# Performance work log

Hardware: AMD Instinct MI355X
Metric: run time of the kernel (lower is better)

The kernel has to match this reference:

```python
import jax, jax.numpy as jnp
import numpy as np

DIM = 1024
NUM_HEAD = 16
DIM_HEAD = DIM // NUM_HEAD
RMS_EPS = 1.1920929e-07  # torch.finfo(float32).eps (nn.RMSNorm default eps=None)
EPS_LIN = 1e-6
THETA = 10000.0


def rmsnorm(x, g, eps=RMS_EPS):
    return x * jax.lax.rsqrt(jnp.mean(x * x, axis=-1, keepdims=True) + eps) * g


def rope_cos_sin(seq_len, dim_head, dtype=jnp.float32):
    inv_freq = 1.0 / (THETA ** (jnp.arange(0, dim_head, 2, dtype=dtype) / dim_head))
    t = jnp.arange(seq_len, dtype=dtype)
    freqs = jnp.outer(t, inv_freq)  # [L, dh//2]
    return jnp.cos(freqs), jnp.sin(freqs)


def apply_rope(t, cos, sin):
    # t: [b, h, L, dh]; pairs are (t[...,2i], t[...,2i+1]) viewed as complex
    tr = t[..., 0::2]
    ti = t[..., 1::2]
    out_r = tr * cos - ti * sin
    out_i = tr * sin + ti * cos
    return jnp.stack([out_r, out_i], axis=-1).reshape(t.shape)


def setup_inputs() -> dict:
    key = jax.random.key(0)
    ks = jax.random.split(key, 5)
    B, L = 4, 4096
    x = jax.random.normal(ks[0], (B, L, DIM), dtype=jnp.float32)
    Wqkv = jax.random.normal(ks[1], (3 * DIM, DIM), dtype=jnp.float32) * 0.02
    bqkv = jax.random.normal(ks[2], (3 * DIM,), dtype=jnp.float32) * 0.02
    gq = jnp.ones((DIM,), dtype=jnp.float32)
    gk = jnp.ones((DIM,), dtype=jnp.float32)
    Wout = jax.random.normal(ks[3], (DIM, DIM), dtype=jnp.float32) * 0.02
    bout = jax.random.normal(ks[4], (DIM,), dtype=jnp.float32) * 0.02
    gout = jnp.ones((DIM,), dtype=jnp.float32)
    return {"x": x, "Wqkv": Wqkv, "bqkv": bqkv, "gq": gq, "gk": gk,
            "Wout": Wout, "bout": bout, "gout": gout}


def reference(x, Wqkv, bqkv, gq, gk, Wout, bout, gout):
    B, L, D = x.shape
    qkv = x @ Wqkv.T + bqkv  # [B, L, 3D]
    q, k, v = jnp.split(qkv, 3, axis=-1)
    q = rmsnorm(q, gq)
    k = rmsnorm(k, gk)
    # b L (h d) -> b h L d
    split = lambda t: t.reshape(B, L, NUM_HEAD, DIM_HEAD).transpose(0, 2, 1, 3)
    q, k, v = split(q), split(k), split(v)
    cos, sin = rope_cos_sin(L, DIM_HEAD)  # start_pos = 0 (default)
    cos = cos[None, None]  # [1,1,L,dh//2]
    sin = sin[None, None]
    q = apply_rope(q, cos, sin)
    k = apply_rope(k, cos, sin)
    # linear attention: ReLU feature map + padded-value normalization trick
    qf = jax.nn.relu(q)
    kf = jax.nn.relu(k)
    vpad = jnp.concatenate([v, jnp.ones_like(v[..., :1])], axis=-1)  # pad_val=1.0
    vk = jnp.einsum('bhlp,bhld->bhpd', vpad, kf)       # [b,h,dh+1,dh]
    res = jnp.einsum('bhpd,bhld->bhlp', vk, qf)        # [b,h,L,dh+1]
    attn = res[..., :-1] / (res[..., -1:] + EPS_LIN)
    attn = attn.transpose(0, 2, 1, 3).reshape(B, L, D)  # b h L d -> b L (h d)
    out = rmsnorm(attn @ Wout.T + bout, gout)
    return out
```

## Files before the change

kernel.cpp:

```cpp
#include <hip/hip_runtime.h>
#include <stdint.h>

#define RMS_EPS 1.1920929e-07f
#define EPS_LIN 1e-6f

typedef __attribute__((ext_vector_type(8))) short bf16x8;
typedef __attribute__((ext_vector_type(4))) float f32x4;

__device__ __forceinline__ unsigned short f2bf(float f) {
  union { float f; unsigned int u; } v; v.f = f;
  unsigned int r = v.u + 0x7fffu + ((v.u >> 16) & 1u);
  return (unsigned short)(r >> 16);
}
__device__ __forceinline__ float bf2f(unsigned short s) {
  union { unsigned int u; float f; } v; v.u = ((unsigned int)s) << 16;
  return v.f;
}

__global__ __launch_bounds__(256) void k_init(
    const float* __restrict__ x, const float* __restrict__ Wqkv,
    const float* __restrict__ Wout,
    unsigned short* __restrict__ xb, unsigned short* __restrict__ wqkvb,
    unsigned short* __restrict__ woutb,
    float* __restrict__ cosT, float* __restrict__ sinT,
    float* __restrict__ vkbuf) {
  const int blk = blockIdx.x;
  const int t = threadIdx.x;
  if (blk < 20480) {
    const float* src;
    unsigned short* dst;
    int base;
    if (blk < 16384) { src = x; dst = xb; base = blk; }
    else if (blk < 19456) { src = Wqkv; dst = wqkvb; base = blk - 16384; }
    else { src = Wout; dst = woutb; base = blk - 19456; }
    int i = (base * 256 + t) * 4;
    float4 v = *reinterpret_cast<const float4*>(src + i);
    ushort4 o = { f2bf(v.x), f2bf(v.y), f2bf(v.z), f2bf(v.w) };
    *reinterpret_cast<ushort4*>(dst + i) = o;
  } else if (blk < 20992) {
    int idx = (blk - 20480) * 256 + t;
    int l = idx >> 5, i = idx & 31;
    float inv_freq = expf(-((float)(2 * i) / 64.0f) * logf(10000.0f));
    float ang = (float)l * inv_freq;
    cosT[idx] = cosf(ang);
    sinT[idx] = sinf(ang);
  } else {
    int i = ((blk - 20992) * 256 + t) * 4;
    if (i < 64 * 65 * 64) {
      float4 z = { 0.f, 0.f, 0.f, 0.f };
      *reinterpret_cast<float4*>(vkbuf + i) = z;
    }
  }
}

__device__ __forceinline__ void stage16(const unsigned short* g, unsigned short* lds_base,
                                        int lane) {
#if __has_builtin(__builtin_amdgcn_global_load_lds)
  __builtin_amdgcn_global_load_lds(
      (const __attribute__((address_space(1))) unsigned int*)g,
      (__attribute__((address_space(3))) unsigned int*)lds_base, 16, 0, 0);
#else
  *reinterpret_cast<uint4*>(lds_base + lane * 8) = *reinterpret_cast<const uint4*>(g);
#endif
}

__global__ __launch_bounds__(256, 3) void k_gemm_bt(
    const unsigned short* __restrict__ A, const unsigned short* __restrict__ Bw,
    const float* __restrict__ bias, int M, int N, int K, int mode,
    unsigned short* __restrict__ qb, unsigned short* __restrict__ kb,
    unsigned short* __restrict__ vb, unsigned short* __restrict__ preb) {
  __shared__ unsigned short As[128 * 64];
  __shared__ unsigned short Bs[128 * 64];
  const int nt = N >> 7;
  const int bm = blockIdx.x / nt, bn = blockIdx.x % nt;
  const int m0 = bm << 7, n0 = bn << 7;
  const int t = threadIdx.x;
  const int wave = t >> 6, lane = t & 63;
  const int wr = wave >> 1, wc = wave & 1;
  const int quad = lane >> 4, m16 = lane & 15;

  const unsigned short* ApS[4];
  const unsigned short* BpS[4];
  unsigned short* AlS[4];
  unsigned short* BlS[4];
#pragma unroll
  for (int s = 0; s < 4; ++s) {
    int u = wave * 256 + s * 64 + lane;
    int row = u >> 3;
    int ku = (u & 7) ^ (row & 7);
    ApS[s] = A + (size_t)(m0 + row) * K + ku * 8;
    BpS[s] = Bw + (size_t)(n0 + row) * K + ku * 8;
    AlS[s] = As + (size_t)(wave * 256 + s * 64) * 8;
    BlS[s] = Bs + (size_t)(wave * 256 + s * 64) * 8;
  }

  int offA[4][2], offB[4][2];
#pragma unroll
  for (int i = 0; i < 4; ++i) {
    int rowA = wr * 64 + i * 16 + m16;
    int rowB = wc * 64 + i * 16 + m16;
#pragma unroll
    for (int ks = 0; ks < 2; ++ks) {
      int kuf = ks * 4 + quad;
      offA[i][ks] = (rowA * 8 + (kuf ^ (rowA & 7))) * 8;
      offB[i][ks] = (rowB * 8 + (kuf ^ (rowB & 7))) * 8;
    }
  }

  f32x4 acc[4][4] = {};

  for (int k0 = 0; k0 < K; k0 += 64) {
#pragma unroll
    for (int s = 0; s < 4; ++s) {
      stage16(ApS[s] + k0, AlS[s], lane);
      stage16(BpS[s] + k0, BlS[s], lane);
    }
    __syncthreads();
#pragma unroll
    for (int ks = 0; ks < 2; ++ks) {
      bf16x8 fa[4], fb[4];
#pragma unroll
      for (int i = 0; i < 4; ++i)
        fa[i] = *reinterpret_cast<const bf16x8*>(As + offA[i][ks]);
#pragma unroll
      for (int j = 0; j < 4; ++j)
        fb[j] = *reinterpret_cast<const bf16x8*>(Bs + offB[j][ks]);
#pragma unroll
      for (int i = 0; i < 4; ++i)
#pragma unroll
        for (int j = 0; j < 4; ++j)
          acc[i][j] = __builtin_amdgcn_mfma_f32_16x16x32_bf16(fa[i], fb[j], acc[i][j], 0, 0, 0);
    }
    __syncthreads();
  }

#pragma unroll
  for (int i = 0; i < 4; ++i) {
    int rbase = m0 + wr * 64 + i * 16 + quad * 4;
#pragma unroll
    for (int j = 0; j < 4; ++j) {
      int col = n0 + wc * 64 + j * 16 + m16;
      float bc = bias[col];
#pragma unroll
      for (int r = 0; r < 4; ++r) {
        int row = rbase + r;
        float val = acc[i][j][r] + bc;
        unsigned short bv = f2bf(val);
        if (mode == 0) {
          if (col < 1024) {
            qb[(size_t)row * 1024 + col] = bv;
          } else if (col < 2048) {
            kb[(size_t)row * 1024 + (col - 1024)] = bv;
          } else {
            int h = (col - 2048) >> 6, d = col & 63;
            int b = row >> 12, l = row & 4095;
            vb[(((size_t)(b * 16 + h)) * 4096 + l) * 64 + d] = bv;
          }
        } else {
          preb[(size_t)row * N + col] = bv;
        }
      }
    }
  }
}

__global__ __launch_bounds__(256) void k_qknorm(
    const unsigned short* __restrict__ qb, const unsigned short* __restrict__ kb,
    const float* __restrict__ gq, const float* __restrict__ gk,
    const float* __restrict__ cosT, const float* __restrict__ sinT,
    unsigned short* __restrict__ qfb, unsigned short* __restrict__ kfb) {
  const int wid = (blockIdx.x << 2) + (threadIdx.x >> 6);
  const int row = wid >> 1;
  const int which = wid & 1;
  const int lane = threadIdx.x & 63;
  const int l = row & 4095;
  const int b = row >> 12;
  const unsigned short* src = (which ? kb : qb) + (size_t)row * 1024;
  const float* g = which ? gk : gq;
  unsigned short* dstb = which ? kfb : qfb;

  float v[16];
  float ss = 0.f;
#pragma unroll
  for (int c = 0; c < 4; ++c) {
    int d = c * 256 + lane * 4;
    ushort4 u = *reinterpret_cast<const ushort4*>(src + d);
    float a0 = bf2f(u.x), a1 = bf2f(u.y), a2 = bf2f(u.z), a3 = bf2f(u.w);
    v[c * 4 + 0] = a0; v[c * 4 + 1] = a1; v[c * 4 + 2] = a2; v[c * 4 + 3] = a3;
    ss += a0 * a0 + a1 * a1 + a2 * a2 + a3 * a3;
  }
#pragma unroll
  for (int off = 1; off < 64; off <<= 1) ss += __shfl_xor(ss, off, 64);
  const float sc = rsqrtf(ss * (1.0f / 1024.0f) + RMS_EPS);

#pragma unroll
  for (int c = 0; c < 4; ++c) {
    int d = c * 256 + lane * 4;
    int i0 = (d & 63) >> 1;
    float c0 = cosT[l * 32 + i0], s0 = sinT[l * 32 + i0];
    float c1 = cosT[l * 32 + i0 + 1], s1 = sinT[l * 32 + i0 + 1];
    float x0 = v[c * 4 + 0] * sc * g[d];
    float x1 = v[c * 4 + 1] * sc * g[d + 1];
    float x2 = v[c * 4 + 2] * sc * g[d + 2];
    float x3 = v[c * 4 + 3] * sc * g[d + 3];
    float r0 = x0 * c0 - x1 * s0, r1 = x0 * s0 + x1 * c0;
    float r2 = x2 * c1 - x3 * s1, r3 = x2 * s1 + x3 * c1;
    ushort4 o = { f2bf(fmaxf(r0, 0.f)), f2bf(fmaxf(r1, 0.f)),
                  f2bf(fmaxf(r2, 0.f)), f2bf(fmaxf(r3, 0.f)) };
    int h = d >> 6;
    *reinterpret_cast<ushort4*>(dstb + (((size_t)(b * 16 + h)) * 4096 + l) * 64 + (d & 63)) = o;
  }
}

__global__ __launch_bounds__(256) void k_vk(const unsigned short* __restrict__ vb,
                                            const unsigned short* __restrict__ kfb,
                                            float* __restrict__ vk) {
  const int bh = blockIdx.x >> 4;
  const int chunk = blockIdx.x & 15;
  const int t = threadIdx.x;
  const int wv = t >> 6, tx = t & 63;
  __shared__ float vt[64 * 64];
  __shared__ float kt[64 * 64];
  float acc[16] = {};
  float accD = 0.f;
  const int lb = chunk * 256;
  for (int tile = 0; tile < 4; ++tile) {
    const size_t rowbase = ((size_t)bh * 4096 + lb + tile * 64) * 64;
#pragma unroll
    for (int r = 0; r < 4; ++r) {
      int e = r * 1024 + t * 4;
      ushort4 uv = *reinterpret_cast<const ushort4*>(vb + rowbase + e);
      ushort4 uk = *reinterpret_cast<const ushort4*>(kfb + rowbase + e);
      float4 fv = { bf2f(uv.x), bf2f(uv.y), bf2f(uv.z), bf2f(uv.w) };
      float4 fk = { bf2f(uk.x), bf2f(uk.y), bf2f(uk.z), bf2f(uk.w) };
      *reinterpret_cast<float4*>(vt + e) = fv;
      *reinterpret_cast<float4*>(kt + e) = fk;
    }
    __syncthreads();
#pragma unroll 4
    for (int lp = 0; lp < 64; ++lp) {
      float kvv = kt[lp * 64 + tx];
      const float4* vr = reinterpret_cast<const float4*>(vt + lp * 64 + wv * 16);
      float4 v0 = vr[0], v1 = vr[1], v2 = vr[2], v3 = vr[3];
      acc[0] += v0.x * kvv;  acc[1] += v0.y * kvv;
      acc[2] += v0.z * kvv;  acc[3] += v0.w * kvv;
      acc[4] += v1.x * kvv;  acc[5] += v1.y * kvv;
      acc[6] += v1.z * kvv;  acc[7] += v1.w * kvv;
      acc[8] += v2.x * kvv;  acc[9] += v2.y * kvv;
      acc[10] += v2.z * kvv; acc[11] += v2.w * kvv;
      acc[12] += v3.x * kvv; acc[13] += v3.y * kvv;
      acc[14] += v3.z * kvv; acc[15] += v3.w * kvv;
      accD += kvv;
    }
    __syncthreads();
  }
  float* dst = vk + (size_t)bh * 65 * 64;
#pragma unroll
  for (int pp = 0; pp < 16; ++pp) atomicAdd(dst + (wv * 16 + pp) * 64 + tx, acc[pp]);
  if (wv == 0) atomicAdd(dst + 64 * 64 + tx, accD);
}

__global__ __launch_bounds__(256) void k_res(const unsigned short* __restrict__ qfb,
                                             const float* __restrict__ vk,
                                             unsigned short* __restrict__ attnb) {
  const int bh = blockIdx.x >> 5;
  const int lt = (blockIdx.x & 31) << 7;
  const int b = bh >> 4, h = bh & 15;
  const int t = threadIdx.x;
  const int wave = t >> 6, lane = t & 63;
  __shared__ unsigned short Aq[128 * 64];
  __shared__ unsigned short Bv[64 * 64];
  __shared__ float vkD[64];
  __shared__ float invden[128];

  const unsigned short* Ag = qfb + ((size_t)bh * 4096 + lt) * 64;
#pragma unroll
  for (int s = 0; s < 4; ++s)
    stage16(Ag + wave * 2048 + s * 512 + lane * 8, Aq + wave * 2048 + s * 512, lane);

  const float* vsrc = vk + (size_t)bh * 65 * 64;
  {
    int base = t * 16;
#pragma unroll
    for (int c = 0; c < 4; ++c) {
      float4 f = *reinterpret_cast<const float4*>(vsrc + base + c * 4);
      ushort4 o = { f2bf(f.x), f2bf(f.y), f2bf(f.z), f2bf(f.w) };
      *reinterpret_cast<ushort4*>(Bv + base + c * 4) = o;
    }
  }
  if (t < 64) vkD[t] = vsrc[64 * 64 + t];
  __syncthreads();

  f32x4 acc[2][4] = {};
  const int quad = lane >> 4, m16 = lane & 15;
#pragma unroll
  for (int step = 0; step < 2; ++step) {
    bf16x8 fa[2], fb[4];
#pragma unroll
    for (int i = 0; i < 2; ++i)
      fa[i] = *reinterpret_cast<const bf16x8*>(Aq + (wave * 32 + i * 16 + m16) * 64 +
                                               step * 32 + quad * 8);
#pragma unroll
    for (int j = 0; j < 4; ++j)
      fb[j] = *reinterpret_cast<const bf16x8*>(Bv + (j * 16 + m16) * 64 +
                                               step * 32 + quad * 8);
#pragma unroll
    for (int i = 0; i < 2; ++i)
#pragma unroll
      for (int j = 0; j < 4; ++j)
        acc[i][j] = __builtin_amdgcn_mfma_f32_16x16x32_bf16(fa[i], fb[j], acc[i][j], 0, 0, 0);
  }

  {
    const unsigned short* qr = Aq + (t >> 1) * 64 + (t & 1) * 32;
    const float* vd = vkD + (t & 1) * 32;
    float ds = 0.f;
#pragma unroll
    for (int c = 0; c < 4; ++c) {
      bf16x8 qv = *reinterpret_cast<const bf16x8*>(qr + c * 8);
#pragma unroll
      for (int j = 0; j < 8; ++j)
        ds += bf2f((unsigned short)qv[j]) * vd[c * 8 + j];
    }
    ds += __shfl_xor(ds, 1, 64);
    if ((t & 1) == 0) invden[t >> 1] = 1.0f / (ds + EPS_LIN);
  }
  __syncthreads();

#pragma unroll
  for (int i = 0; i < 2; ++i) {
#pragma unroll
    for (int r = 0; r < 4; ++r) {
      int row = wave * 32 + i * 16 + quad * 4 + r;
      float inv = invden[row];
      unsigned short* dst = attnb + ((size_t)(b * 4096 + lt + row)) * 1024 + h * 64;
#pragma unroll
      for (int j = 0; j < 4; ++j)
        dst[j * 16 + m16] = f2bf(acc[i][j][r] * inv);
    }
  }
}

__global__ __launch_bounds__(256) void k_outnorm(const unsigned short* __restrict__ preb,
                                                 const float* __restrict__ gout,
                                                 float* __restrict__ out) {
  const int row = (blockIdx.x << 2) + (threadIdx.x >> 6);
  const int lane = threadIdx.x & 63;
  const unsigned short* src = preb + (size_t)row * 1024;
  float* drow = out + (size_t)row * 1024;
  float v[16];
  float ss = 0.f;
#pragma unroll
  for (int c = 0; c < 4; ++c) {
    int d = c * 256 + lane * 4;
    ushort4 u = *reinterpret_cast<const ushort4*>(src + d);
    float a0 = bf2f(u.x), a1 = bf2f(u.y), a2 = bf2f(u.z), a3 = bf2f(u.w);
    v[c * 4 + 0] = a0; v[c * 4 + 1] = a1; v[c * 4 + 2] = a2; v[c * 4 + 3] = a3;
    ss += a0 * a0 + a1 * a1 + a2 * a2 + a3 * a3;
  }
#pragma unroll
  for (int off = 1; off < 64; off <<= 1) ss += __shfl_xor(ss, off, 64);
  const float sc = rsqrtf(ss * (1.0f / 1024.0f) + RMS_EPS);
#pragma unroll
  for (int c = 0; c < 4; ++c) {
    int d = c * 256 + lane * 4;
    float4 o = { v[c * 4 + 0] * sc * gout[d], v[c * 4 + 1] * sc * gout[d + 1],
                 v[c * 4 + 2] * sc * gout[d + 2], v[c * 4 + 3] * sc * gout[d + 3] };
    *reinterpret_cast<float4*>(drow + d) = o;
  }
}

#define OFF_XB     0ull
#define OFF_WQKVB  33554432ull
#define OFF_WOUTB  39845888ull
#define OFF_QB     41943040ull
#define OFF_KB     75497472ull
#define OFF_VB     109051904ull
#define OFF_QFB    142606336ull
#define OFF_KFB    176160768ull
#define OFF_VK     209715200ull
#define OFF_ATTNB  210780160ull
#define OFF_COST   244334592ull
#define OFF_SINT   244858880ull
#define WS_NEEDED  245383168ull

extern "C" void kernel_launch(void* const* d_in, const int* in_sizes, int n_in,
                              void* d_out, int out_size, void* d_ws, size_t ws_size,
                              hipStream_t stream) {
  const float* x    = (const float*)d_in[0];
  const float* Wqkv = (const float*)d_in[1];
  const float* bqkv = (const float*)d_in[2];
  const float* gq   = (const float*)d_in[3];
  const float* gk   = (const float*)d_in[4];
  const float* Wout = (const float*)d_in[5];
  const float* bout = (const float*)d_in[6];
  const float* gout = (const float*)d_in[7];

  if (ws_size < WS_NEEDED) return;

  char* ws = (char*)d_ws;
  unsigned short* xb    = (unsigned short*)(ws + OFF_XB);
  unsigned short* wqkvb = (unsigned short*)(ws + OFF_WQKVB);
  unsigned short* woutb = (unsigned short*)(ws + OFF_WOUTB);
  unsigned short* qb    = (unsigned short*)(ws + OFF_QB);
  unsigned short* kb    = (unsigned short*)(ws + OFF_KB);
  unsigned short* vb    = (unsigned short*)(ws + OFF_VB);
  unsigned short* qfb   = (unsigned short*)(ws + OFF_QFB);
  unsigned short* kfb   = (unsigned short*)(ws + OFF_KFB);
  float*          vkbuf = (float*)(ws + OFF_VK);
  unsigned short* attnb = (unsigned short*)(ws + OFF_ATTNB);
  float*          cosT  = (float*)(ws + OFF_COST);
  float*          sinT  = (float*)(ws + OFF_SINT);
  unsigned short* preb  = (unsigned short*)(ws + OFF_QB);

  k_init<<<21252, 256, 0, stream>>>(x, Wqkv, Wout, xb, wqkvb, woutb, cosT, sinT, vkbuf);

  k_gemm_bt<<<128 * 24, 256, 0, stream>>>(xb, wqkvb, bqkv, 16384, 3072, 1024, 0,
                                          qb, kb, vb, nullptr);
  k_qknorm<<<8192, 256, 0, stream>>>(qb, kb, gq, gk, cosT, sinT, qfb, kfb);

  k_vk<<<1024, 256, 0, stream>>>(vb, kfb, vkbuf);
  k_res<<<2048, 256, 0, stream>>>(qfb, vkbuf, attnb);

  k_gemm_bt<<<128 * 8, 256, 0, stream>>>(attnb, woutb, bout, 16384, 1024, 1024, 1,
                                         nullptr, nullptr, nullptr, preb);
  k_outnorm<<<4096, 256, 0, stream>>>(preb, gout, (float*)d_out);
}
```

Baseline: 395.1 us.

## Restructure vk reduction into per-wave 8x8 register outer-product tiles

The k_vk kernel now gives each wave its own slice of sequence rows. Each lane accumulates an 8x8 register tile of the V^T·K outer product, fed by vectorized LDS loads, instead of a 16x1 strip per thread. Partial tiles from the four waves are summed in shared memory before global atomics, so each block issues fewer atomic adds. The grid is halved, so each block covers 512 rows. This trades more registers per thread and an extra LDS reduction pass for higher arithmetic intensity per LDS load.

```diff
diff --git a/kernel.cpp b/kernel.cpp
--- a/kernel.cpp
+++ b/kernel.cpp
@@ -212,52 +212,99 @@
   }
 }
 
+__device__ __forceinline__ float4 lo4(uint4 u) {
+  union { unsigned int v; float f; } a0, a1, b0, b1;
+  a0.v = u.x << 16; a1.v = u.x & 0xffff0000u;
+  b0.v = u.y << 16; b1.v = u.y & 0xffff0000u;
+  float4 r = { a0.f, a1.f, b0.f, b1.f };
+  return r;
+}
+__device__ __forceinline__ float4 hi4(uint4 u) {
+  union { unsigned int v; float f; } a0, a1, b0, b1;
+  a0.v = u.z << 16; a1.v = u.z & 0xffff0000u;
+  b0.v = u.w << 16; b1.v = u.w & 0xffff0000u;
+  float4 r = { a0.f, a1.f, b0.f, b1.f };
+  return r;
+}
+
 __global__ __launch_bounds__(256) void k_vk(const unsigned short* __restrict__ vb,
                                             const unsigned short* __restrict__ kfb,
                                             float* __restrict__ vk) {
-  const int bh = blockIdx.x >> 4;
-  const int chunk = blockIdx.x & 15;
+  const int bh = blockIdx.x >> 3;
+  const int chunk = blockIdx.x & 7;
   const int t = threadIdx.x;
-  const int wv = t >> 6, tx = t & 63;
-  __shared__ float vt[64 * 64];
-  __shared__ float kt[64 * 64];
-  float acc[16] = {};
-  float accD = 0.f;
-  const int lb = chunk * 256;
-  for (int tile = 0; tile < 4; ++tile) {
-    const size_t rowbase = ((size_t)bh * 4096 + lb + tile * 64) * 64;
-#pragma unroll
-    for (int r = 0; r < 4; ++r) {
-      int e = r * 1024 + t * 4;
-      ushort4 uv = *reinterpret_cast<const ushort4*>(vb + rowbase + e);
-      ushort4 uk = *reinterpret_cast<const ushort4*>(kfb + rowbase + e);
-      float4 fv = { bf2f(uv.x), bf2f(uv.y), bf2f(uv.z), bf2f(uv.w) };
-      float4 fk = { bf2f(uk.x), bf2f(uk.y), bf2f(uk.z), bf2f(uk.w) };
-      *reinterpret_cast<float4*>(vt + e) = fv;
-      *reinterpret_cast<float4*>(kt + e) = fk;
+  const int wv = t >> 6, lane = t & 63;
+  const int p0 = (lane >> 3) << 3, d0 = (lane & 7) << 3;
+  __shared__ float sh[16384];
+  float* vt = sh + wv * 2048;
+  float* kt = sh + 8192 + wv * 2048;
+
+  float acc[8][8] = {};
+  float accD[8] = {};
+
+  for (int it = 0; it < 4; ++it) {
+    const int l0 = (chunk * 16 + wv * 4 + it) * 32;
+    const size_t base = ((size_t)bh * 4096 + l0) * 64;
+#pragma unroll
+    for (int c = 0; c < 4; ++c) {
+      const int e = c * 512 + lane * 8;
+      uint4 uv = *reinterpret_cast<const uint4*>(vb + base + e);
+      uint4 uk = *reinterpret_cast<const uint4*>(kfb + base + e);
+      *reinterpret_cast<float4*>(vt + e) = lo4(uv);
+      *reinterpret_cast<float4*>(vt + e + 4) = hi4(uv);
+      *reinterpret_cast<float4*>(kt + e) = lo4(uk);
+      *reinterpret_cast<float4*>(kt + e + 4) = hi4(uk);
     }
     __syncthreads();
-#pragma unroll 4
-    for (int lp = 0; lp < 64; ++lp) {
-      float kvv = kt[lp * 64 + tx];
-      const float4* vr = reinterpret_cast<const float4*>(vt + lp * 64 + wv * 16);
-      float4 v0 = vr[0], v1 = vr[1], v2 = vr[2], v3 = vr[3];
-      acc[0] += v0.x * kvv;  acc[1] += v0.y * kvv;
-      acc[2] += v0.z * kvv;  acc[3] += v0.w * kvv;
-      acc[4] += v1.x * kvv;  acc[5] += v1.y * kvv;
-      acc[6] += v1.z * kvv;  acc[7] += v1.w * kvv;
-      acc[8] += v2.x * kvv;  acc[9] += v2.y * kvv;
-      acc[10] += v2.z * kvv; acc[11] += v2.w * kvv;
-      acc[12] += v3.x * kvv; acc[13] += v3.y * kvv;
-      acc[14] += v3.z * kvv; acc[15] += v3.w * kvv;
-      accD += kvv;
+#pragma unroll 2
+    for (int lp = 0; lp < 32; ++lp) {
+      const float* vr = vt + lp * 64 + p0;
+      const float* kr = kt + lp * 64 + d0;
+      float4 v0 = *reinterpret_cast<const float4*>(vr);
+      float4 v1 = *reinterpret_cast<const float4*>(vr + 4);
+      float4 k0 = *reinterpret_cast<const float4*>(kr);
+      float4 k1 = *reinterpret_cast<const float4*>(kr + 4);
+      float vv[8] = { v0.x, v0.y, v0.z, v0.w, v1.x, v1.y, v1.z, v1.w };
+      float kk[8] = { k0.x, k0.y, k0.z, k0.w, k1.x, k1.y, k1.z, k1.w };
+#pragma unroll
+      for (int i = 0; i < 8; ++i)
+#pragma unroll
+        for (int j = 0; j < 8; ++j)
+          acc[i][j] += vv[i] * kk[j];
+#pragma unroll
+      for (int j = 0; j < 8; ++j) accD[j] += kk[j];
     }
     __syncthreads();
   }
+
+  float* reg = sh + wv * 4096;
+#pragma unroll
+  for (int i = 0; i < 8; ++i) {
+    float4 lo = { acc[i][0], acc[i][1], acc[i][2], acc[i][3] };
+    float4 hi = { acc[i][4], acc[i][5], acc[i][6], acc[i][7] };
+    *reinterpret_cast<float4*>(reg + (p0 + i) * 64 + d0) = lo;
+    *reinterpret_cast<float4*>(reg + (p0 + i) * 64 + d0 + 4) = hi;
+  }
+  __syncthreads();
   float* dst = vk + (size_t)bh * 65 * 64;
 #pragma unroll
-  for (int pp = 0; pp < 16; ++pp) atomicAdd(dst + (wv * 16 + pp) * 64 + tx, acc[pp]);
-  if (wv == 0) atomicAdd(dst + 64 * 64 + tx, accD);
+  for (int q = 0; q < 4; ++q) {
+    const int o = t * 16 + q * 4;
+    float4 s = *reinterpret_cast<const float4*>(sh + o);
+#pragma unroll
+    for (int w = 1; w < 4; ++w) {
+      float4 r = *reinterpret_cast<const float4*>(sh + w * 4096 + o);
+      s.x += r.x; s.y += r.y; s.z += r.z; s.w += r.w;
+    }
+    atomicAdd(dst + o + 0, s.x);
+    atomicAdd(dst + o + 1, s.y);
+    atomicAdd(dst + o + 2, s.z);
+    atomicAdd(dst + o + 3, s.w);
+  }
+  if (lane < 8) {
+#pragma unroll
+    for (int j = 0; j < 8; ++j) atomicAdd(dst + 64 * 64 + d0 + j, accD[j]);
+  }
 }
 
 __global__ __launch_bounds__(256) void k_res(const unsigned short* __restrict__ qfb,
@@ -419,7 +466,7 @@
                                           qb, kb, vb, nullptr);
   k_qknorm<<<8192, 256, 0, stream>>>(qb, kb, gq, gk, cosT, sinT, qfb, kfb);
 
-  k_vk<<<1024, 256, 0, stream>>>(vb, kfb, vkbuf);
+  k_vk<<<512, 256, 0, stream>>>(vb, kfb, vkbuf);
   k_res<<<2048, 256, 0, stream>>>(qfb, vkbuf, attnb);
 
   k_gemm_bt<<<128 * 8, 256, 0, stream>>>(attnb, woutb, bout, 16384, 1024, 1024, 1,
```

After: 485.0 us. 22.8% more time.

## Compute V^T K with bf16 MFMA and replace atomics with a partial-sum reduction kernel

Applied to the files above, without the earlier changes.

Rewrites the per-head V^T·K accumulation to stage transposed bf16 tiles in LDS and use 16x16x32 bf16 MFMA instead of scalar FP32 FMAs. The atomicAdd accumulation across 16 sequence chunks is replaced by writing per-chunk partials into a scratch buffer (aliased onto the attention output region) and summing them in a new small reduction kernel. This is meant to cut ALU time and atomic contention, at the cost of an extra launch, extra global traffic for the partials, and strided scalar loads during staging.

```diff
diff --git a/kernel.cpp b/kernel.cpp
--- a/kernel.cpp
+++ b/kernel.cpp
@@ -214,50 +214,67 @@
 
 __global__ __launch_bounds__(256) void k_vk(const unsigned short* __restrict__ vb,
                                             const unsigned short* __restrict__ kfb,
-                                            float* __restrict__ vk) {
+                                            float* __restrict__ part) {
   const int bh = blockIdx.x >> 4;
   const int chunk = blockIdx.x & 15;
   const int t = threadIdx.x;
-  const int wv = t >> 6, tx = t & 63;
-  __shared__ float vt[64 * 64];
-  __shared__ float kt[64 * 64];
-  float acc[16] = {};
+  const int wv = t >> 6, lane = t & 63;
+  const int quad = lane >> 4, m16 = lane & 15;
+
+  __shared__ __align__(16) unsigned short Vt[64 * 40];
+  __shared__ __align__(16) unsigned short Kt[64 * 40];
+  __shared__ float dred[4][64];
+
+  f32x4 acc[4] = {};
   float accD = 0.f;
-  const int lb = chunk * 256;
-  for (int tile = 0; tile < 4; ++tile) {
-    const size_t rowbase = ((size_t)bh * 4096 + lb + tile * 64) * 64;
-#pragma unroll
-    for (int r = 0; r < 4; ++r) {
-      int e = r * 1024 + t * 4;
-      ushort4 uv = *reinterpret_cast<const ushort4*>(vb + rowbase + e);
-      ushort4 uk = *reinterpret_cast<const ushort4*>(kfb + rowbase + e);
-      float4 fv = { bf2f(uv.x), bf2f(uv.y), bf2f(uv.z), bf2f(uv.w) };
-      float4 fk = { bf2f(uk.x), bf2f(uk.y), bf2f(uk.z), bf2f(uk.w) };
-      *reinterpret_cast<float4*>(vt + e) = fv;
-      *reinterpret_cast<float4*>(kt + e) = fk;
-    }
+
+  for (int tile = 0; tile < 8; ++tile) {
+    const size_t rbase =
+        ((size_t)bh * 4096 + chunk * 256 + tile * 32 + wv * 8) * 64 + lane;
+    bf16x8 vv, kv;
+#pragma unroll
+    for (int j = 0; j < 8; ++j) {
+      unsigned short ve = vb[rbase + j * 64];
+      unsigned short ke = kfb[rbase + j * 64];
+      vv[j] = (short)ve;
+      kv[j] = (short)ke;
+      accD += bf2f(ke);
+    }
+    *reinterpret_cast<bf16x8*>(Vt + lane * 40 + wv * 8) = vv;
+    *reinterpret_cast<bf16x8*>(Kt + lane * 40 + wv * 8) = kv;
     __syncthreads();
-#pragma unroll 4
-    for (int lp = 0; lp < 64; ++lp) {
-      float kvv = kt[lp * 64 + tx];
-      const float4* vr = reinterpret_cast<const float4*>(vt + lp * 64 + wv * 16);
-      float4 v0 = vr[0], v1 = vr[1], v2 = vr[2], v3 = vr[3];
-      acc[0] += v0.x * kvv;  acc[1] += v0.y * kvv;
-      acc[2] += v0.z * kvv;  acc[3] += v0.w * kvv;
-      acc[4] += v1.x * kvv;  acc[5] += v1.y * kvv;
-      acc[6] += v1.z * kvv;  acc[7] += v1.w * kvv;
-      acc[8] += v2.x * kvv;  acc[9] += v2.y * kvv;
-      acc[10] += v2.z * kvv; acc[11] += v2.w * kvv;
-      acc[12] += v3.x * kvv; acc[13] += v3.y * kvv;
-      acc[14] += v3.z * kvv; acc[15] += v3.w * kvv;
-      accD += kvv;
+
+    bf16x8 fa = *reinterpret_cast<const bf16x8*>(Vt + (wv * 16 + m16) * 40 + quad * 8);
+#pragma unroll
+    for (int j = 0; j < 4; ++j) {
+      bf16x8 fb = *reinterpret_cast<const bf16x8*>(Kt + (j * 16 + m16) * 40 + quad * 8);
+      acc[j] = __builtin_amdgcn_mfma_f32_16x16x32_bf16(fa, fb, acc[j], 0, 0, 0);
     }
     __syncthreads();
   }
-  float* dst = vk + (size_t)bh * 65 * 64;
-#pragma unroll
-  for (int pp = 0; pp < 16; ++pp) atomicAdd(dst + (wv * 16 + pp) * 64 + tx, acc[pp]);
-  if (wv == 0) atomicAdd(dst + 64 * 64 + tx, accD);
+
+  float* dst = part + ((size_t)chunk * 64 + bh) * 4160;
+#pragma unroll
+  for (int j = 0; j < 4; ++j)
+#pragma unroll
+    for (int r = 0; r < 4; ++r)
+      dst[(wv * 16 + quad * 4 + r) * 64 + j * 16 + m16] = acc[j][r];
+
+  dred[wv][lane] = accD;
+  __syncthreads();
+  if (t < 64) dst[64 * 64 + t] = dred[0][t] + dred[1][t] + dred[2][t] + dred[3][t];
+}
+
+__global__ __launch_bounds__(256) void k_vkred(const float* __restrict__ part,
+                                               float* __restrict__ vk) {
+  const int i = (blockIdx.x * 256 + threadIdx.x) * 4;
+  float4 s = *reinterpret_cast<const float4*>(part + i);
+#pragma unroll
+  for (int c = 1; c < 16; ++c) {
+    float4 r = *reinterpret_cast<const float4*>(part + (size_t)c * 266240 + i);
+    s.x += r.x; s.y += r.y; s.z += r.z; s.w += r.w;
+  }
+  *reinterpret_cast<float4*>(vk + i) = s;
 }
 
 __global__ __launch_bounds__(256) void k_res(const unsigned short* __restrict__ qfb,
@@ -412,6 +429,7 @@
   float*          cosT  = (float*)(ws + OFF_COST);
   float*          sinT  = (float*)(ws + OFF_SINT);
   unsigned short* preb  = (unsigned short*)(ws + OFF_QB);
+  float*          vkpart = (float*)(ws + OFF_ATTNB);
 
   k_init<<<21252, 256, 0, stream>>>(x, Wqkv, Wout, xb, wqkvb, woutb, cosT, sinT, vkbuf);
 
@@ -419,7 +437,9 @@
                                           qb, kb, vb, nullptr);
   k_qknorm<<<8192, 256, 0, stream>>>(qb, kb, gq, gk, cosT, sinT, qfb, kfb);
 
-  k_vk<<<1024, 256, 0, stream>>>(vb, kfb, vkbuf);
+  k_vk<<<1024, 256, 0, stream>>>(vb, kfb, vkpart);
+  k_vkred<<<260, 256, 0, stream>>>(vkpart, vkbuf);
+
   k_res<<<2048, 256, 0, stream>>>(qfb, vkbuf, attnb);
 
   k_gemm_bt<<<128 * 8, 256, 0, stream>>>(attnb, woutb, bout, 16384, 1024, 1024, 1,
```

Result: faster. 370.4 us (-6.2%).
